# Optimization experiments

Hardware: AMD Instinct MI355X
Metric: run time of the kernel (lower is better)

## Reference

```python
import jax, jax.numpy as jnp
import numpy as np

T, B, D, H = 64, 512, 768, 12
HD = D // H
EPS = 1e-8  # torch cosine_similarity eps


def setup_inputs() -> dict:
    key = jax.random.key(0)
    k0, k1, k2, k3 = jax.random.split(key, 4)
    node_embs = jax.random.normal(k0, (T, B, D), dtype=jnp.float32)
    in_proj_w = jax.random.normal(k1, (3 * D, D), dtype=jnp.float32) * 0.02
    in_proj_b = jnp.zeros((3 * D,), dtype=jnp.float32)
    out_proj_w = jax.random.normal(k2, (D, D), dtype=jnp.float32) * 0.02
    out_proj_b = jnp.zeros((D,), dtype=jnp.float32)
    return {"node_embs": node_embs, "in_proj_w": in_proj_w, "in_proj_b": in_proj_b,
            "out_proj_w": out_proj_w, "out_proj_b": out_proj_b}


def reference(node_embs, in_proj_w, in_proj_b, out_proj_w, out_proj_b):
    # node_embs: (T, B, D). Original loops over t calling MHA on (B, 1, D)
    # i.e. self-attention across the B axis with batch=1, fused here over T.
    qkv = jnp.einsum('tbd,ed->tbe', node_embs, in_proj_w) + in_proj_b  # (T, B, 3D)
    q, k, v = jnp.split(qkv, 3, axis=-1)

    def heads(x):  # (T, B, D) -> (T, H, B, HD)
        return x.reshape(T, B, H, HD).transpose(0, 2, 1, 3)

    q, k, v = heads(q), heads(k), heads(v)
    scores = jnp.einsum('thqd,thkd->thqk', q, k) / np.sqrt(HD).astype(np.float32)
    attn = jax.nn.softmax(scores, axis=-1)
    ctx = jnp.einsum('thqk,thkd->thqd', attn, v)  # (T, H, B, HD)
    ctx = ctx.transpose(0, 2, 1, 3).reshape(T, B, D)
    out = jnp.einsum('tbd,ed->tbe', ctx, out_proj_w) + out_proj_b  # (T, B, D)

    # cosine similarity between all pairs over B, then mean over first index
    norm = jnp.maximum(jnp.linalg.norm(out, axis=-1), EPS)  # (T, B)
    xn = out / norm[..., None]
    sim = jnp.einsum('tid,tjd->tij', xn, xn)  # (T, B, B)
    adj = sim.mean(axis=1)[..., None]  # (T, B, 1) == (T, B, N) with N=1
    return adj
```

## Files before the change

### kernel.cpp

```cpp
#include <hip/hip_runtime.h>

#define T_ 64
#define B_ 512
#define D_ 768
#define H_ 12
#define HD_ 64
#define M1 (T_*B_)
#define N_QKV (3*D_)

typedef __attribute__((ext_vector_type(8))) short short8;
typedef __attribute__((ext_vector_type(4))) float f32x4;

__device__ __forceinline__ unsigned short f2b(float f) {
  unsigned int u = __float_as_uint(f);
  u = (u + 0x7FFFu + ((u >> 16) & 1u)) >> 16;
  return (unsigned short)u;
}
__device__ __forceinline__ float b2f(unsigned short s) {
  return __uint_as_float(((unsigned int)s) << 16);
}

__device__ __forceinline__ void load_lds16(const unsigned short* g, unsigned short* l) {
  __builtin_amdgcn_global_load_lds(
      (const __attribute__((address_space(1))) unsigned int*)g,
      (__attribute__((address_space(3))) unsigned int*)l, 16, 0, 0);
}

#define N4_NODE 6291456
#define N4_WQKV 442368
#define N4_WOUT 147456
__global__ __launch_bounds__(256) void k_cast_all(
    const float* __restrict__ node, const float* __restrict__ wqkv,
    const float* __restrict__ wout, unsigned short* __restrict__ x_bf,
    unsigned short* __restrict__ wqkv_bf, unsigned short* __restrict__ wout_bf) {
  int i = blockIdx.x * 256 + threadIdx.x;
  const float* src; unsigned short* dst; int off;
  if (i < N4_NODE)                 { src = node; dst = x_bf;    off = i; }
  else if (i < N4_NODE + N4_WQKV)  { src = wqkv; dst = wqkv_bf; off = i - N4_NODE; }
  else                             { src = wout; dst = wout_bf; off = i - N4_NODE - N4_WQKV; }
  float4 v = ((const float4*)src)[off];
  ushort4 o;
  o.x = f2b(v.x); o.y = f2b(v.y); o.z = f2b(v.z); o.w = f2b(v.w);
  ((ushort4*)dst)[off] = o;
}

#define SB0() __builtin_amdgcn_sched_barrier(0)
#define BARF() do { SB0(); __builtin_amdgcn_s_barrier(); SB0(); } while (0)
#define WLG0() asm volatile("s_waitcnt lgkmcnt(0)" ::: "memory")
#define WVM4() asm volatile("s_waitcnt vmcnt(4)" ::: "memory")
#define WVM0() asm volatile("s_waitcnt vmcnt(0)" ::: "memory")

#define STG(SLOT, GOFF) do { \
  load_lds16(Ag  + (GOFF),          lds + (SLOT)*16384 + tid*8); \
  load_lds16(Ag  + 98304 + (GOFF),  lds + (SLOT)*16384 + 4096 + tid*8); \
  load_lds16(Bg0 + (GOFF),          lds + (SLOT)*16384 + 8192 + tid*8); \
  load_lds16(Bg0 + 98304 + (GOFF),  lds + (SLOT)*16384 + 12288 + tid*8); \
} while (0)

#define RD(GU) do { \
  const unsigned short* ga_ = lds + (GU)*16384; \
  _Pragma("unroll") \
  for (int mf = 0; mf < 8; mf++) aF[mf] = *(const short8*)(ga_ + aBase + mf*512); \
  _Pragma("unroll") \
  for (int nf = 0; nf < 4; nf++) bF[nf] = *(const short8*)(ga_ + bBase + nf*512); \
} while (0)

#define MM() do { \
  __builtin_amdgcn_s_setprio(1); \
  _Pragma("unroll") \
  for (int mf = 0; mf < 8; mf++) \
    _Pragma("unroll") \
    for (int nf = 0; nf < 4; nf++) \
      acc[mf][nf] = __builtin_amdgcn_mfma_f32_16x16x32_bf16(aF[mf], bF[nf], acc[mf][nf], 0, 0, 0); \
  __builtin_amdgcn_s_setprio(0); \
} while (0)

#define PHASE(GU, SSLOT, GOFF) do { RD(GU); STG(SSLOT, GOFF); WVM4(); WLG0(); MM(); BARF(); } while (0)

#define GEMM_RING_KLOOP(Aptr, Bptr) \
  const int tid = threadIdx.x; \
  const int lane = tid & 63, wave = tid >> 6; \
  const int ln = lane & 15, quad = lane >> 4; \
  const int wm = wave & 1, wn = wave >> 1; \
   \
  const int w_ = tid & 7, g_ = tid >> 3; \
  const int rowS_ = ((g_ >> 2) << 3) + (w_ & 4) + (g_ & 3); \
  const int octS_ = (w_ & 3) ^ (g_ & 3); \
  const unsigned short* Ag = Aptr + (size_t)(m0 + rowS_)*768 + octS_*8; \
  const unsigned short* Bg0 = Bptr + (size_t)(n0 + rowS_)*768 + octS_*8; \
   \
  const int inner_ = (((ln>>3)*4 + (ln&3))*8 + ((ln&7) ^ quad)) * 8; \
  const int aBase = wm*4096 + inner_; \
  const int bBase = 8192 + (wn>>1)*4096 + (wn&1)*2048 + inner_; \
  short8 aF[8], bF[4]; \
  f32x4 acc[8][4] = {}; \
  STG(0, 0); STG(1, 32); \
  WVM4(); BARF(); \
  for (int J = 0; J < 7; ++J) { \
    PHASE(0, 2, 64); PHASE(1, 0, 96); PHASE(2, 1, 128); \
    Ag += 96; Bg0 += 96; \
  } \
   \
  RD(0); STG(2, 64); WVM4(); WLG0(); MM(); BARF(); \
  RD(1); WVM0(); WLG0(); MM(); BARF(); \
  RD(2); WLG0(); MM(); \
  __syncthreads();

__global__ __launch_bounds__(512, 2) void k_gemm_qkv8(
    const unsigned short* __restrict__ A,
    const unsigned short* __restrict__ Bw,
    const float* __restrict__ bias,
    unsigned short* __restrict__ qo,
    unsigned short* __restrict__ ko,
    unsigned short* __restrict__ vTo)
{
  extern __shared__ __align__(16) unsigned short lds[];
  const int bb = blockIdx.x;
  const int xcd = bb & 7, idx = bb >> 3;
  const int m0 = (xcd*16 + idx/9) * 256;
  const int n0 = (idx%9) * 256;
  GEMM_RING_KLOOP(A, Bw)

  const int t = m0 >> 9, mb = m0 & 511;
  if (n0 < 1536) {
    unsigned short* dst = (n0 < 768) ? qo : ko;
    const int colbase = (n0 < 768) ? n0 : n0 - 768;
#pragma unroll
    for (int half = 0; half < 2; half++) {
      __syncthreads();
      if (wm == half) {
#pragma unroll
        for (int nf = 0; nf < 4; nf++) {
          const int col = wn*64 + nf*16 + ln;
          const float bi = bias[n0 + col];
          const int cc = col >> 3, cs = col & 7;
#pragma unroll
          for (int mf = 0; mf < 8; mf++) {
            const int row = mf*16 + quad*4;
#pragma unroll
            for (int r = 0; r < 4; r++) {
              const int rw = row + r;
              lds[rw*256 + ((cc ^ (rw&7))<<3) + cs] = f2b(acc[mf][nf][r] + bi);
            }
          }
        }
      }
      __syncthreads();
#pragma unroll
      for (int it = 0; it < 8; it++) {
        int ci = it*512 + tid;
        int r2 = ci >> 5, cj = ci & 31;
        int within = colbase + cj*8;
        int h = within >> 6, hd = within & 63;
        *(uint4*)&dst[((size_t)(t*H_ + h)*B_ + mb + half*128 + r2)*HD_ + hd] =
            *(const uint4*)&lds[r2*256 + ((cj ^ (r2&7))<<3)];
      }
    }
  } else {
#pragma unroll
    for (int ch = 0; ch < 2; ch++) {
      __syncthreads();
      if ((wn >> 1) == ch) {
#pragma unroll
        for (int nf = 0; nf < 4; nf++) {
          const int col = wn*64 + nf*16 + ln;
          const int cl = col & 127;
          const float bi = bias[n0 + col];
#pragma unroll
          for (int mf = 0; mf < 8; mf++) {
            const int row = wm*128 + mf*16 + quad*4;
            ushort4 pk;
            pk.x = f2b(acc[mf][nf][0] + bi);
            pk.y = f2b(acc[mf][nf][1] + bi);
            pk.z = f2b(acc[mf][nf][2] + bi);
            pk.w = f2b(acc[mf][nf][3] + bi);
            *(ushort4*)&lds[cl*256 + (((row>>3) ^ (cl&7))<<3) + (row&7)] = pk;
          }
        }
      }
      __syncthreads();
#pragma unroll
      for (int it = 0; it < 8; it++) {
        int ci = it*512 + tid;
        int r2 = ci >> 5, cj = ci & 31;
        int cg = (n0 - 1536) + ch*128 + r2;
        int h = cg >> 6, hd = cg & 63;
        *(uint4*)&vTo[((size_t)(t*H_ + h)*HD_ + hd)*B_ + mb + cj*8] =
            *(const uint4*)&lds[r2*256 + ((cj ^ (r2&7))<<3)];
      }
    }
  }
}

__global__ __launch_bounds__(512, 2) void k_gemm_out8(
    const unsigned short* __restrict__ A,
    const unsigned short* __restrict__ Bw,
    const float* __restrict__ bias,
    unsigned short* __restrict__ outb)
{
  extern __shared__ __align__(16) unsigned short lds[];
  const int bb = blockIdx.x;
  const int xcd = bb & 7, idx = bb >> 3;
  const int m0 = (xcd*16 + idx/3) * 256;
  const int n0 = (idx%3) * 256;
  GEMM_RING_KLOOP(A, Bw)

#pragma unroll
  for (int half = 0; half < 2; half++) {
    __syncthreads();
    if (wm == half) {
#pragma unroll
      for (int nf = 0; nf < 4; nf++) {
        const int col = wn*64 + nf*16 + ln;
        const float bi = bias[n0 + col];
        const int cc = col >> 3, cs = col & 7;
#pragma unroll
        for (int mf = 0; mf < 8; mf++) {
          const int row = mf*16 + quad*4;
#pragma unroll
          for (int r = 0; r < 4; r++) {
            const int rw = row + r;
            lds[rw*256 + ((cc ^ (rw&7))<<3) + cs] = f2b(acc[mf][nf][r] + bi);
          }
        }
      }
    }
    __syncthreads();
#pragma unroll
    for (int it = 0; it < 8; it++) {
      int ci = it*512 + tid;
      int r2 = ci >> 5, cj = ci & 31;
      *(uint4*)&outb[(size_t)(m0 + half*128 + r2)*768 + n0 + cj*8] =
          *(const uint4*)&lds[r2*256 + ((cj ^ (r2&7))<<3)];
    }
  }
}

__global__ __launch_bounds__(512) void k_attn(
    const unsigned short* __restrict__ q,
    const unsigned short* __restrict__ k,
    const unsigned short* __restrict__ vT,
    unsigned short* __restrict__ ctx)
{
  __shared__ __align__(16) unsigned short Ks[64*64];
  __shared__ __align__(16) unsigned short VT[64*64];
  __shared__ __align__(16) unsigned short Ps[8*32*72];
  __shared__ float Dn[8*64];
  const int tid = threadIdx.x;
  const int lane = tid & 63, wave = tid >> 6;
  const int ln = lane & 15, quad = lane >> 4;
  const int pxr = 8 * (ln >> 2);
  const int bb = blockIdx.x;
  const int xcd = bb & 7, idx = bb >> 3;
  const int th = xcd*96 + (idx >> 1);
  const int q0 = (idx & 1) * 256;
  const int t = th / H_, h = th - t*H_;
  const size_t base  = (size_t)th * (B_*HD_);
  const size_t baseT = (size_t)th * (HD_*B_);

  short8 qf[2][2];
#pragma unroll
  for (int s = 0; s < 2; s++) {
    const unsigned short* qp = &q[base + (size_t)(q0 + wave*32 + s*16 + ln)*HD_ + quad*8];
    qf[s][0] = *(const short8*)qp;
    qf[s][1] = *(const short8*)(qp + 32);
  }
  f32x4 acc[2][4] = {};
  float dpart[2] = {0.f, 0.f};
  unsigned short* Pw = &Ps[wave*32*72];

  for (int kt = 0; kt < B_; kt += 64) {
    __syncthreads();
    {
      int s = tid;
      int r = s >> 3, cp = s & 7, c = cp ^ (r & 7);
      load_lds16(&k[base + (size_t)(kt + r)*HD_ + c*8], &Ks[s*8]);
      load_lds16(&vT[baseT + (size_t)r*B_ + kt + c*8], &VT[s*8]);
    }
    __syncthreads();
    f32x4 sf[2][4] = {};
#pragma unroll
    for (int ki = 0; ki < 4; ki++) {
      int row = ki*16 + ln;
      short8 kf0 = *(const short8*)&Ks[row*64 + (quad     ^ (row & 7))*8];
      short8 kf1 = *(const short8*)&Ks[row*64 + ((4+quad) ^ (row & 7))*8];
#pragma unroll
      for (int s = 0; s < 2; s++) {
        sf[s][ki] = __builtin_amdgcn_mfma_f32_16x16x32_bf16(kf0, qf[s][0], sf[s][ki], 0, 0, 0);
        sf[s][ki] = __builtin_amdgcn_mfma_f32_16x16x32_bf16(kf1, qf[s][1], sf[s][ki], 0, 0, 0);
      }
    }
#pragma unroll
    for (int s = 0; s < 2; s++)
#pragma unroll
      for (int ki = 0; ki < 4; ki++) {
        float p0 = __expf(sf[s][ki][0] * 0.125f);
        float p1 = __expf(sf[s][ki][1] * 0.125f);
        float p2 = __expf(sf[s][ki][2] * 0.125f);
        float p3 = __expf(sf[s][ki][3] * 0.125f);
        dpart[s] += (p0 + p1) + (p2 + p3);
        uint2 uu;
        uu.x = (__float_as_uint(p1) & 0xFFFF0000u) | (__float_as_uint(p0) >> 16);
        uu.y = (__float_as_uint(p3) & 0xFFFF0000u) | (__float_as_uint(p2) >> 16);
        int col = (ki*16 + quad*4) ^ pxr;
        *(uint2*)&Pw[(s*16 + ln)*72 + col] = uu;
      }
    short8 pa[2][2];
#pragma unroll
    for (int s = 0; s < 2; s++)
#pragma unroll
      for (int hf = 0; hf < 2; hf++)
        pa[s][hf] = *(const short8*)&Pw[(s*16 + ln)*72 + ((hf*32 + quad*8) ^ pxr)];
#pragma unroll
    for (int ds = 0; ds < 4; ds++) {
      int row = ds*16 + ln;
      short8 vb0 = *(const short8*)&VT[row*64 + (quad     ^ (row & 7))*8];
      short8 vb1 = *(const short8*)&VT[row*64 + ((4+quad) ^ (row & 7))*8];
#pragma unroll
      for (int s = 0; s < 2; s++) {
        acc[s][ds] = __builtin_amdgcn_mfma_f32_16x16x32_bf16(pa[s][0], vb0, acc[s][ds], 0, 0, 0);
        acc[s][ds] = __builtin_amdgcn_mfma_f32_16x16x32_bf16(pa[s][1], vb1, acc[s][ds], 0, 0, 0);
      }
    }
  }
#pragma unroll
  for (int s = 0; s < 2; s++) {
    float d = dpart[s];
    d += __shfl_xor(d, 16);
    d += __shfl_xor(d, 32);
    if (quad == 0) Dn[wave*64 + s*16 + ln] = d;
  }
#pragma unroll
  for (int s = 0; s < 2; s++) {
    int qrow = q0 + wave*32 + s*16 + quad*4;
#pragma unroll
    for (int r = 0; r < 4; r++) {
      float invd = 1.f / Dn[wave*64 + s*16 + quad*4 + r];
      size_t o = ((size_t)t*B_ + (qrow + r))*D_ + h*HD_ + ln;
#pragma unroll
      for (int ds = 0; ds < 4; ds++)
        ctx[o + ds*16] = f2b(acc[s][ds][r] * invd);
    }
  }
}

__global__ __launch_bounds__(256) void k_norms1(const unsigned short* __restrict__ outb,
                                                float* __restrict__ norms,
                                                float* __restrict__ pmvec)
{
  __shared__ float wsum[4*768];
  int blk = blockIdx.x;
  int t = blk >> 3, c = blk & 7;
  int wave = threadIdx.x >> 6, lane = threadIdx.x & 63;
  float macc[12];
#pragma unroll
  for (int j = 0; j < 12; j++) macc[j] = 0.f;
  for (int i = 0; i < 16; i++) {
    int b = c*64 + wave*16 + i;
    const unsigned short* row = &outb[((size_t)t*B_ + b)*D_];
    float x[12]; float ss = 0.f;
#pragma unroll
    for (int j = 0; j < 12; j++) { x[j] = b2f(row[lane + 64*j]); ss += x[j]*x[j]; }
#pragma unroll
    for (int off = 32; off; off >>= 1) ss += __shfl_xor(ss, off);
    float nr = fmaxf(sqrtf(ss), 1e-8f);
    if (lane == 0) norms[(size_t)t*B_ + b] = nr;
    float inv = 1.f / nr;
#pragma unroll
    for (int j = 0; j < 12; j++) macc[j] += x[j]*inv;
  }
#pragma unroll
  for (int j = 0; j < 12; j++) wsum[wave*768 + 64*j + lane] = macc[j];
  __syncthreads();
  for (int d = threadIdx.x; d < 768; d += 256) {
    pmvec[(size_t)blk*768 + d] = wsum[d] + wsum[768 + d] + wsum[1536 + d] + wsum[2304 + d];
  }
}

__global__ __launch_bounds__(256) void k_norms2(const float* __restrict__ pmvec,
                                                float* __restrict__ mvec)
{
  int t = blockIdx.x;
  for (int d = threadIdx.x; d < 768; d += 256) {
    float s = 0.f;
#pragma unroll
    for (int c = 0; c < 8; c++) s += pmvec[(size_t)(t*8 + c)*768 + d];
    mvec[t*768 + d] = s * (1.0f/512.0f);
  }
}

__global__ __launch_bounds__(256) void k_adj(const unsigned short* __restrict__ outb,
                                             const float* __restrict__ norms,
                                             const float* __restrict__ mvec,
                                             float* __restrict__ adj)
{
  int idx = blockIdx.x*4 + (threadIdx.x >> 6);
  int lane = threadIdx.x & 63;
  int t = idx >> 9;
  const unsigned short* row = &outb[(size_t)idx*768];
  const float* m = &mvec[t*768];
  float dot = 0.f;
#pragma unroll
  for (int j = 0; j < 12; j++) dot += b2f(row[lane + 64*j]) * m[lane + 64*j];
#pragma unroll
  for (int off = 32; off; off >>= 1) dot += __shfl_xor(dot, off);
  if (lane == 0) adj[idx] = dot / norms[idx];
}

extern "C" void kernel_launch(void* const* d_in, const int* in_sizes, int n_in,
                              void* d_out, int out_size, void* d_ws, size_t ws_size,
                              hipStream_t stream)
{
  const float* node = (const float*)d_in[0];
  const float* wqkv = (const float*)d_in[1];
  const float* bqkv = (const float*)d_in[2];
  const float* wout = (const float*)d_in[3];
  const float* bout = (const float*)d_in[4];
  float* adj = (float*)d_out;

  char* ws = (char*)d_ws;
  const size_t SZ = (size_t)M1*D_*2;
  unsigned short* q_bf    = (unsigned short*)(ws);
  unsigned short* k_bf    = (unsigned short*)(ws + SZ);
  unsigned short* vT_bf   = (unsigned short*)(ws + 2*SZ);
  unsigned short* ctx_bf  = (unsigned short*)(ws + 3*SZ);
  unsigned short* x_bf    = (unsigned short*)(ws + 4*SZ);
  unsigned short* wqkv_bf = (unsigned short*)(ws + 5*SZ);
  unsigned short* wout_bf = (unsigned short*)(ws + 5*SZ + 3538944);
  unsigned short* out_bf  = (unsigned short*)(ws);
  float* pmvec            = (float*)(ws + 4*SZ);
  float* norms            = (float*)(ws + 5*SZ + 3538944 + 1179648);
  float* mvec             = (float*)(ws + 5*SZ + 3538944 + 1179648 + 131072);

  static int shmem_set = 0;
  if (!shmem_set) {
    hipFuncSetAttribute((const void*)k_gemm_qkv8,
                        hipFuncAttributeMaxDynamicSharedMemorySize, 98304);
    hipFuncSetAttribute((const void*)k_gemm_out8,
                        hipFuncAttributeMaxDynamicSharedMemorySize, 98304);
    shmem_set = 1;
  }

  k_cast_all<<<26880, 256, 0, stream>>>(node, wqkv, wout, x_bf, wqkv_bf, wout_bf);
  k_gemm_qkv8<<<1152, 512, 98304, stream>>>(x_bf, wqkv_bf, bqkv, q_bf, k_bf, vT_bf);
  k_attn<<<1536, 512, 0, stream>>>(q_bf, k_bf, vT_bf, ctx_bf);
  k_gemm_out8<<<384, 512, 98304, stream>>>(ctx_bf, wout_bf, bout, out_bf);
  k_norms1<<<T_*8, 256, 0, stream>>>(out_bf, norms, pmvec);
  k_norms2<<<T_, 256, 0, stream>>>(pmvec, mvec);
  k_adj<<<M1/4, 256, 0, stream>>>(out_bf, norms, mvec, adj);
}
```

Measured before the change: 452.0 us.

## Deepen GEMM LDS ring to four slots and split MFMA phases into halves

Reworks the shared GEMM k-loop used by the QKV and output projections to prefetch three k-tiles ahead into a 4-slot LDS ring. Each k-step is split into two half-phases, so LDS fragment reads of the next A half overlap with MFMAs on the current half, and A and B global loads are staged in separate halves. The goal is to hide global-load and LDS-read latency better. In exchange it raises dynamic LDS to 128KB per block, which may reduce occupancy, and adds more barriers per k-step.

```diff
diff --git a/kernel.cpp b/kernel.cpp
--- a/kernel.cpp
+++ b/kernel.cpp
@@ -47,35 +47,67 @@
 #define SB0() __builtin_amdgcn_sched_barrier(0)
 #define BARF() do { SB0(); __builtin_amdgcn_s_barrier(); SB0(); } while (0)
 #define WLG0() asm volatile("s_waitcnt lgkmcnt(0)" ::: "memory")
+#define WVM8() asm volatile("s_waitcnt vmcnt(8)" ::: "memory")
+#define WVM6() asm volatile("s_waitcnt vmcnt(6)" ::: "memory")
 #define WVM4() asm volatile("s_waitcnt vmcnt(4)" ::: "memory")
 #define WVM0() asm volatile("s_waitcnt vmcnt(0)" ::: "memory")
 
-#define STG(SLOT, GOFF) do { \
-  load_lds16(Ag  + (GOFF),          lds + (SLOT)*16384 + tid*8); \
-  load_lds16(Ag  + 98304 + (GOFF),  lds + (SLOT)*16384 + 4096 + tid*8); \
+#define STG_A(SLOT, GOFF) do { \
+  load_lds16(Ag + (GOFF),          lds + (SLOT)*16384 + tid*8); \
+  load_lds16(Ag + 98304 + (GOFF),  lds + (SLOT)*16384 + 4096 + tid*8); \
+} while (0)
+#define STG_B(SLOT, GOFF) do { \
   load_lds16(Bg0 + (GOFF),          lds + (SLOT)*16384 + 8192 + tid*8); \
   load_lds16(Bg0 + 98304 + (GOFF),  lds + (SLOT)*16384 + 12288 + tid*8); \
 } while (0)
 
-#define RD(GU) do { \
-  const unsigned short* ga_ = lds + (GU)*16384; \
-  _Pragma("unroll") \
-  for (int mf = 0; mf < 8; mf++) aF[mf] = *(const short8*)(ga_ + aBase + mf*512); \
-  _Pragma("unroll") \
-  for (int nf = 0; nf < 4; nf++) bF[nf] = *(const short8*)(ga_ + bBase + nf*512); \
-} while (0)
-
-#define MM() do { \
+#define RD_ALO(PAR, SLOT) do { \
+  const unsigned short* p_ = lds + (SLOT)*16384 + aBase; \
+  aLo[PAR][0] = *(const short8*)(p_); \
+  aLo[PAR][1] = *(const short8*)(p_ + 512); \
+  aLo[PAR][2] = *(const short8*)(p_ + 1024); \
+  aLo[PAR][3] = *(const short8*)(p_ + 1536); \
+} while (0)
+
+#define RD_BHI(SLOT) do { \
+  const unsigned short* pb_ = lds + (SLOT)*16384 + bBase; \
+  bC[0] = *(const short8*)(pb_); \
+  bC[1] = *(const short8*)(pb_ + 512); \
+  bC[2] = *(const short8*)(pb_ + 1024); \
+  bC[3] = *(const short8*)(pb_ + 1536); \
+  const unsigned short* pa_ = lds + (SLOT)*16384 + aBase + 2048; \
+  aHi[0] = *(const short8*)(pa_); \
+  aHi[1] = *(const short8*)(pa_ + 512); \
+  aHi[2] = *(const short8*)(pa_ + 1024); \
+  aHi[3] = *(const short8*)(pa_ + 1536); \
+} while (0)
+
+#define MM_LO(PAR) do { \
   __builtin_amdgcn_s_setprio(1); \
   _Pragma("unroll") \
-  for (int mf = 0; mf < 8; mf++) \
+  for (int mf = 0; mf < 4; mf++) \
     _Pragma("unroll") \
     for (int nf = 0; nf < 4; nf++) \
-      acc[mf][nf] = __builtin_amdgcn_mfma_f32_16x16x32_bf16(aF[mf], bF[nf], acc[mf][nf], 0, 0, 0); \
+      acc[mf][nf] = __builtin_amdgcn_mfma_f32_16x16x32_bf16(aLo[PAR][mf], bC[nf], acc[mf][nf], 0, 0, 0); \
   __builtin_amdgcn_s_setprio(0); \
 } while (0)
 
-#define PHASE(GU, SSLOT, GOFF) do { RD(GU); STG(SSLOT, GOFF); WVM4(); WLG0(); MM(); BARF(); } while (0)
+#define MM_HI() do { \
+  __builtin_amdgcn_s_setprio(1); \
+  _Pragma("unroll") \
+  for (int mf = 0; mf < 4; mf++) \
+    _Pragma("unroll") \
+    for (int nf = 0; nf < 4; nf++) \
+      acc[4+mf][nf] = __builtin_amdgcn_mfma_f32_16x16x32_bf16(aHi[mf], bC[nf], acc[4+mf][nf], 0, 0, 0); \
+  __builtin_amdgcn_s_setprio(0); \
+} while (0)
+
+#define P0(SLOT, PAR, SSLOT, GOFF, WVSTMT) do { \
+  RD_BHI(SLOT); STG_A(SSLOT, GOFF); WVSTMT; BARF(); WLG0(); MM_LO(PAR); BARF(); \
+} while (0)
+#define P1(NPAR, NSLOT, SSLOT, GOFF) do { \
+  RD_ALO(NPAR, NSLOT); STG_B(SSLOT, GOFF); BARF(); MM_HI(); BARF(); \
+} while (0)
 
 #define GEMM_RING_KLOOP(Aptr, Bptr) \
   const int tid = threadIdx.x; \
@@ -92,18 +124,36 @@
   const int inner_ = (((ln>>3)*4 + (ln&3))*8 + ((ln&7) ^ quad)) * 8; \
   const int aBase = wm*4096 + inner_; \
   const int bBase = 8192 + (wn>>1)*4096 + (wn&1)*2048 + inner_; \
-  short8 aF[8], bF[4]; \
+  short8 aLo[2][4], aHi[4], bC[4]; \
   f32x4 acc[8][4] = {}; \
-  STG(0, 0); STG(1, 32); \
-  WVM4(); BARF(); \
-  for (int J = 0; J < 7; ++J) { \
-    PHASE(0, 2, 64); PHASE(1, 0, 96); PHASE(2, 1, 128); \
-    Ag += 96; Bg0 += 96; \
+  STG_A(0, 0); STG_B(0, 0); STG_A(1, 32); STG_B(1, 32); STG_A(2, 64); STG_B(2, 64); \
+  WVM8(); BARF(); \
+  RD_ALO(0, 0); \
+   \
+  P0(0, 0, 3, 96, WVM6()); \
+  P1(1, 1, 3, 96); \
+  for (int J = 0; J < 5; ++J) { \
+     \
+    P0(1, 1, 0, 128, WVM6()); \
+    P1(0, 2, 0, 128); \
+     \
+    P0(2, 0, 1, 160, WVM6()); \
+    P1(1, 3, 1, 160); \
+     \
+    P0(3, 1, 2, 192, WVM6()); \
+    P1(0, 0, 2, 192); \
+     \
+    P0(0, 0, 3, 224, WVM6()); \
+    P1(1, 1, 3, 224); \
+    Ag += 128; Bg0 += 128; \
   } \
    \
-  RD(0); STG(2, 64); WVM4(); WLG0(); MM(); BARF(); \
-  RD(1); WVM0(); WLG0(); MM(); BARF(); \
-  RD(2); WLG0(); MM(); \
+  RD_BHI(1); WVM4(); BARF(); WLG0(); MM_LO(1); BARF(); \
+  RD_ALO(0, 2); BARF(); MM_HI(); BARF(); \
+  RD_BHI(2); WVM0(); BARF(); WLG0(); MM_LO(0); BARF(); \
+  RD_ALO(1, 3); BARF(); MM_HI(); BARF(); \
+  RD_BHI(3); BARF(); WLG0(); MM_LO(1); BARF(); \
+  MM_HI(); \
   __syncthreads();
 
 __global__ __launch_bounds__(512, 2) void k_gemm_qkv8(
@@ -435,16 +485,16 @@
   static int shmem_set = 0;
   if (!shmem_set) {
     hipFuncSetAttribute((const void*)k_gemm_qkv8,
-                        hipFuncAttributeMaxDynamicSharedMemorySize, 98304);
+                        hipFuncAttributeMaxDynamicSharedMemorySize, 131072);
     hipFuncSetAttribute((const void*)k_gemm_out8,
-                        hipFuncAttributeMaxDynamicSharedMemorySize, 98304);
+                        hipFuncAttributeMaxDynamicSharedMemorySize, 131072);
     shmem_set = 1;
   }
 
   k_cast_all<<<26880, 256, 0, stream>>>(node, wqkv, wout, x_bf, wqkv_bf, wout_bf);
-  k_gemm_qkv8<<<1152, 512, 98304, stream>>>(x_bf, wqkv_bf, bqkv, q_bf, k_bf, vT_bf);
+  k_gemm_qkv8<<<1152, 512, 131072, stream>>>(x_bf, wqkv_bf, bqkv, q_bf, k_bf, vT_bf);
   k_attn<<<1536, 512, 0, stream>>>(q_bf, k_bf, vT_bf, ctx_bf);
-  k_gemm_out8<<<384, 512, 98304, stream>>>(ctx_bf, wout_bf, bout, out_bf);
+  k_gemm_out8<<<384, 512, 131072, stream>>>(ctx_bf, wout_bf, bout, out_bf);
   k_norms1<<<T_*8, 256, 0, stream>>>(out_bf, norms, pmvec);
   k_norms2<<<T_, 256, 0, stream>>>(pmvec, mvec);
   k_adj<<<M1/4, 256, 0, stream>>>(out_bf, norms, mvec, adj);
```

Measured after the change: 442.5 us. 1.02x faster.
